# Performance work log

Hardware: AMD Instinct MI355X
Metric: run time of the kernel (lower is better)

Reference implementation:

```python
import jax, jax.numpy as jnp
import numpy as np

BS, C_IN, NP, NA = 2, 64, 1024, 60
NA_OUT, KS, ANN = 60, 3, 8
C_OUT = 128


def setup_inputs() -> dict:
    key = jax.random.key(0)
    k1, k2, k3, k4 = jax.random.split(key, 4)
    feats = jax.random.normal(k1, (BS, C_IN, NP, NA), dtype=jnp.float32)
    # precomputed anchor-neighbor weights, normalized over the ann axis
    w = jax.random.uniform(k2, (NA_OUT, KS, ANN), dtype=jnp.float32)
    intra_w = w / jnp.sum(w, axis=-1, keepdims=True)
    intra_idx = jax.random.randint(k3, (NA_OUT, KS, ANN), 0, NA)
    # xavier-normal-ish weight for the basic conv, flattened [C_OUT, C_IN*KS]
    W = jax.random.normal(k4, (C_OUT, C_IN * KS), dtype=jnp.float32) * (2.0 / np.sqrt(C_IN * KS + C_OUT))
    bias = jnp.full((1, C_OUT, 1), 0.001, dtype=jnp.float32)
    return {"feats": feats, "intra_w": intra_w, "W": W, "bias": bias, "intra_idx": intra_idx}


def reference(feats, intra_w, W, bias, intra_idx):
    bs, c, npts, na = feats.shape
    na_out, ks, ann = intra_idx.shape
    dim_out = W.shape[0]
    # intra_zpconv_grouping_naive: gather over anchor axis then weighted sum over ann
    g = feats[:, :, :, intra_idx]                      # [b, c, p, o, k, a]
    grouped = jnp.einsum('bcpoka,oka->bckpo', g, intra_w)  # [b, c, ks, p, na_out]
    # BasicZPConv: view to [b, c*ks, p*na_out], W @ x + bias
    x = grouped.reshape(bs, c * ks, npts * na_out)
    out = jnp.einsum('oi,bin->bon', W, x) + bias       # [b, dim_out, p*na_out]
    return out.reshape(bs, dim_out, npts, na_out)
```

## Files before the change

### kernel.cpp

```cpp
#include <hip/hip_runtime.h>

#define NPTS 1024
#define NA   60
#define CIN  64
#define KSZ  3
#define ANN  8
#define COUT 128
#define KD   192

using bf16x8 = __attribute__((ext_vector_type(8))) short;
using f32x4  = __attribute__((ext_vector_type(4))) float;

__device__ __forceinline__ unsigned short f2bf(float f) {
    unsigned int u = __builtin_bit_cast(unsigned int, f);
    u += 0x7FFFu + ((u >> 16) & 1u);
    return (unsigned short)(u >> 16);
}

__global__ void build_tables(const float* __restrict__ intra_w,
                             const float* __restrict__ W,
                             const int*   __restrict__ intra_idx,
                             unsigned short* __restrict__ ws) {
    int f = blockIdx.x * 256 + threadIdx.x;
    if (f < 24576) {
        int j = f & 7, l = (f >> 3) & 63, x = f >> 9;
        int kt = x % 6, mt = x / 6;
        int m  = mt * 16 + (l & 15);
        int ip = kt * 32 + 8 * (l >> 4) + j;
        int c  = ip & 63, ks = ip >> 6;
        ws[f] = f2bf(W[m * KD + c * KSZ + ks]);
    } else if (f < 36864) {
        int f2 = f - 24576;
        int j = f2 & 7, l = (f2 >> 3) & 63;
        int kt = (f2 >> 9) & 1, nt = f2 >> 10;
        int np = nt * 16 + (l & 15);
        int ap = kt * 32 + 8 * (l >> 4) + j;
        float s = 0.f;
        if (np < 180 && ap < 60) {
            int ks = (np >= 120) ? 2 : ((np >= 60) ? 1 : 0);
            int o  = np - 60 * ks;
            const int*   ix = intra_idx + (o * KSZ + ks) * ANN;
            const float* wx = intra_w   + (o * KSZ + ks) * ANN;
            #pragma unroll
            for (int a = 0; a < ANN; a++) s += (ix[a] == ap) ? wx[a] : 0.f;
        }
        ws[f] = f2bf(s);
    }
}

__global__ __launch_bounds__(512, 2)
void intrazp_persist(const float* __restrict__ feats,
                     const float* __restrict__ bias,
                     const unsigned short* __restrict__ ws,
                     float* __restrict__ out) {
    __shared__ __align__(16) unsigned short fsS2[64 * 8 * 64];
    __shared__ __align__(16) unsigned short AsT[64 * 192];

    const int t    = threadIdx.x;
    const int wave = t >> 6, lane = t & 63;
    const int l15  = lane & 15, g = lane >> 4;
    const int x    = blockIdx.x;
    const int b    = x >> 7, pbase = (x & 127) * 8;

    const int wm  = wave & 1, wn = wave >> 1;
    const int h   = wave >> 2, nt2 = wave & 3;

    const unsigned short* Sfrag = ws + 24576;
    bf16x8 Sreg[3][2];
    #pragma unroll
    for (int ni = 0; ni < 3; ni++)
        #pragma unroll
        for (int kt = 0; kt < 2; kt++)
            Sreg[ni][kt] = *(const bf16x8*)(Sfrag + (((3 * wn + ni) * 2 + kt) * 64 + lane) * 8);

    bf16x8 Wreg[4][6];
    #pragma unroll
    for (int m = 0; m < 4; m++)
        #pragma unroll
        for (int kt = 0; kt < 6; kt++)
            Wreg[m][kt] = *(const bf16x8*)(ws + (((h * 4 + m) * 6 + kt) * 64 + lane) * 8);

    float4 bvv[4];
    #pragma unroll
    for (int m = 0; m < 4; m++)
        bvv[m] = *(const float4*)(bias + (h * 4 + m) * 16 + 4 * g);

    {
        const float* fb = feats + (size_t)b * CIN * NPTS * NA + (size_t)pbase * NA;
        #pragma unroll
        for (int r = 0; r < 15; r++) {
            int gid = r * 512 + t;
            int c  = gid / 120, u = gid - c * 120;
            int pt = u / 15,   w = u - pt * 15;
            float4 v = *(const float4*)(fb + (size_t)c * NPTS * NA + pt * NA + w * 4);
            unsigned int lo = (unsigned int)f2bf(v.x) | ((unsigned int)f2bf(v.y) << 16);
            unsigned int hi = (unsigned int)f2bf(v.z) | ((unsigned int)f2bf(v.w) << 16);
            int byte = (c * 1024 + pt * 128 + w * 8) ^ ((c & 7) << 4);
            *(uint2*)((char*)fsS2 + byte) = make_uint2(lo, hi);
        }
        {
            int c = t >> 3, pt = t & 7;
            int byte = (c * 1024 + pt * 128 + 120) ^ ((c & 7) << 4);
            *(uint2*)((char*)fsS2 + byte) = make_uint2(0u, 0u);
        }
        if (t < 192) {
            *(uint2*)((char*)AsT + 60 * 384 + t * 8) = make_uint2(0u, 0u);
        }
    }
    __syncthreads();

    for (int pt = 0; pt < 8; ++pt) {
        bf16x8 a1[2][2];
        #pragma unroll
        for (int mi = 0; mi < 2; mi++) {
            int c = (wm * 2 + mi) * 16 + l15;
            #pragma unroll
            for (int kt = 0; kt < 2; kt++) {
                int byte = (c * 1024 + pt * 128 + kt * 64 + g * 16) ^ ((c & 7) << 4);
                a1[mi][kt] = *(const bf16x8*)((char*)fsS2 + byte);
            }
        }
        #pragma unroll
        for (int ni = 0; ni < 3; ni++) {
            int nt = 3 * wn + ni;
            int np = nt * 16 + l15;
            int ks = (np >= 120) ? 2 : ((np >= 60) ? 1 : 0);
            int o  = np - 60 * ks;
            int sw = (o & 7) << 4;
            int rowbyte = o * 384;
            #pragma unroll
            for (int mi = 0; mi < 2; mi++) {
                f32x4 acc1 = {0.f, 0.f, 0.f, 0.f};
                acc1 = __builtin_amdgcn_mfma_f32_16x16x32_bf16(a1[mi][0], Sreg[ni][0], acc1, 0, 0, 0);
                acc1 = __builtin_amdgcn_mfma_f32_16x16x32_bf16(a1[mi][1], Sreg[ni][1], acc1, 0, 0, 0);
                if (np < 180) {
                    int cbase = (wm * 2 + mi) * 16 + 4 * g;
                    int ipb   = ks * 64 + cbase;
                    unsigned int lo = (unsigned int)f2bf(acc1[0]) | ((unsigned int)f2bf(acc1[1]) << 16);
                    unsigned int hi = (unsigned int)f2bf(acc1[2]) | ((unsigned int)f2bf(acc1[3]) << 16);
                    int byte = (rowbyte + ipb * 2) ^ sw;
                    *(uint2*)((char*)AsT + byte) = make_uint2(lo, hi);
                }
            }
        }

        __syncthreads();

        int o   = nt2 * 16 + l15;
        int swo = (o & 7) << 4, rbo = o * 384;
        bf16x8 bb[6];
        #pragma unroll
        for (int kt = 0; kt < 6; kt++)
            bb[kt] = *(const bf16x8*)((char*)AsT + ((rbo + (kt * 32 + 8 * g) * 2) ^ swo));

        f32x4 acc[4];
        #pragma unroll
        for (int m = 0; m < 4; m++) acc[m] = (f32x4){0.f, 0.f, 0.f, 0.f};
        #pragma unroll
        for (int kt = 0; kt < 6; kt++)
            #pragma unroll
            for (int m = 0; m < 4; m++)
                acc[m] = __builtin_amdgcn_mfma_f32_16x16x32_bf16(Wreg[m][kt], bb[kt], acc[m], 0, 0, 0);

        int p = pbase + pt;
        if (o < NA) {
            const size_t cs = (size_t)NPTS * NA;
            #pragma unroll
            for (int m = 0; m < 4; m++) {
                int cbase = (h * 4 + m) * 16 + 4 * g;
                float* ob = out + (((size_t)b * COUT + cbase) * NPTS + p) * NA + o;
                ob[0 * cs] = acc[m][0] + bvv[m].x;
                ob[1 * cs] = acc[m][1] + bvv[m].y;
                ob[2 * cs] = acc[m][2] + bvv[m].z;
                ob[3 * cs] = acc[m][3] + bvv[m].w;
            }
        }

        __syncthreads();
    }
}

extern "C" void kernel_launch(void* const* d_in, const int* in_sizes, int n_in,
                              void* d_out, int out_size, void* d_ws, size_t ws_size,
                              hipStream_t stream) {
    const float* feats     = (const float*)d_in[0];
    const float* intra_w   = (const float*)d_in[1];
    const float* W         = (const float*)d_in[2];
    const float* bias      = (const float*)d_in[3];
    const int*   intra_idx = (const int*)d_in[4];
    float* out = (float*)d_out;
    unsigned short* ws = (unsigned short*)d_ws;

    build_tables<<<dim3(144), dim3(256), 0, stream>>>(intra_w, W, intra_idx, ws);
    intrazp_persist<<<dim3(256), dim3(512), 0, stream>>>(feats, bias, ws, out);
}
```

Before: 105.2 us.

## Stage fp32 feats into LDS via direct global_load_lds and convert per tile

Replaces the register-staged feats load (global load, bf16 convert, swizzled LDS store) with direct global-to-LDS 16-byte async loads of the raw fp32 tile, issued before the weight and table register loads so they overlap. The bf16 conversion and zero padding move into the per-point inner loop, where each fragment read now takes two float4 LDS loads plus conversion. This doubles LDS use for the feature tile (fp32 instead of bf16), drops the XOR swizzle, and repeats conversion work per read. The extra LDS may lower occupancy and raise bank conflicts.

```diff
diff --git a/kernel.cpp b/kernel.cpp
--- a/kernel.cpp
+++ b/kernel.cpp
@@ -15,6 +15,13 @@
     unsigned int u = __builtin_bit_cast(unsigned int, f);
     u += 0x7FFFu + ((u >> 16) & 1u);
     return (unsigned short)(u >> 16);
+}
+
+__device__ __forceinline__ void gload_lds16(const float* g, void* l) {
+    __builtin_amdgcn_global_load_lds(
+        (const __attribute__((address_space(1))) unsigned int*)g,
+        (__attribute__((address_space(3))) unsigned int*)l,
+        16, 0, 0);
 }
 
 __global__ void build_tables(const float* __restrict__ intra_w,
@@ -53,7 +60,7 @@
                      const float* __restrict__ bias,
                      const unsigned short* __restrict__ ws,
                      float* __restrict__ out) {
-    __shared__ __align__(16) unsigned short fsS2[64 * 8 * 64];
+    __shared__ __align__(16) float fsF[8 * 64 * 60];
     __shared__ __align__(16) unsigned short AsT[64 * 192];
 
     const int t    = threadIdx.x;
@@ -65,6 +72,20 @@
     const int wm  = wave & 1, wn = wave >> 1;
     const int h   = wave >> 2, nt2 = wave & 3;
 
+    {
+        const float* fb = feats + (size_t)b * CIN * NPTS * NA + (size_t)pbase * NA;
+        #pragma unroll
+        for (int r = 0; r < 15; r++) {
+            int rem = r * 64 + lane;
+            int c = rem / 15, w = rem - c * 15;
+            const float* gp = fb + (size_t)c * (NPTS * NA) + wave * NA + w * 4;
+            gload_lds16(gp, (char*)fsF + wave * 15360 + r * 1024);
+        }
+        if (t < 192) {
+            *(uint2*)((char*)AsT + 60 * 384 + t * 8) = make_uint2(0u, 0u);
+        }
+    }
+
     const unsigned short* Sfrag = ws + 24576;
     bf16x8 Sreg[3][2];
     #pragma unroll
@@ -85,28 +106,6 @@
     for (int m = 0; m < 4; m++)
         bvv[m] = *(const float4*)(bias + (h * 4 + m) * 16 + 4 * g);
 
-    {
-        const float* fb = feats + (size_t)b * CIN * NPTS * NA + (size_t)pbase * NA;
-        #pragma unroll
-        for (int r = 0; r < 15; r++) {
-            int gid = r * 512 + t;
-            int c  = gid / 120, u = gid - c * 120;
-            int pt = u / 15,   w = u - pt * 15;
-            float4 v = *(const float4*)(fb + (size_t)c * NPTS * NA + pt * NA + w * 4);
-            unsigned int lo = (unsigned int)f2bf(v.x) | ((unsigned int)f2bf(v.y) << 16);
-            unsigned int hi = (unsigned int)f2bf(v.z) | ((unsigned int)f2bf(v.w) << 16);
-            int byte = (c * 1024 + pt * 128 + w * 8) ^ ((c & 7) << 4);
-            *(uint2*)((char*)fsS2 + byte) = make_uint2(lo, hi);
-        }
-        {
-            int c = t >> 3, pt = t & 7;
-            int byte = (c * 1024 + pt * 128 + 120) ^ ((c & 7) << 4);
-            *(uint2*)((char*)fsS2 + byte) = make_uint2(0u, 0u);
-        }
-        if (t < 192) {
-            *(uint2*)((char*)AsT + 60 * 384 + t * 8) = make_uint2(0u, 0u);
-        }
-    }
     __syncthreads();
 
     for (int pt = 0; pt < 8; ++pt) {
@@ -114,10 +113,22 @@
         #pragma unroll
         for (int mi = 0; mi < 2; mi++) {
             int c = (wm * 2 + mi) * 16 + l15;
+            const float* fsrow = fsF + pt * 3840 + c * 60;
             #pragma unroll
             for (int kt = 0; kt < 2; kt++) {
-                int byte = (c * 1024 + pt * 128 + kt * 64 + g * 16) ^ ((c & 7) << 4);
-                a1[mi][kt] = *(const bf16x8*)((char*)fsS2 + byte);
+                int a0 = kt * 32 + 8 * g;
+                float4 lo = *(const float4*)(fsrow + a0);
+                int ah = a0 + 4;
+                bool pad = (ah >= NA);
+                float4 hi = *(const float4*)(fsrow + (pad ? a0 : ah));
+                bf16x8 v;
+                v[0] = (short)f2bf(lo.x); v[1] = (short)f2bf(lo.y);
+                v[2] = (short)f2bf(lo.z); v[3] = (short)f2bf(lo.w);
+                v[4] = (short)(pad ? 0 : f2bf(hi.x));
+                v[5] = (short)(pad ? 0 : f2bf(hi.y));
+                v[6] = (short)(pad ? 0 : f2bf(hi.z));
+                v[7] = (short)(pad ? 0 : f2bf(hi.w));
+                a1[mi][kt] = v;
             }
         }
         #pragma unroll
```

Result: slower. 108.2 us (+2.9%).
